# Performance work log

Hardware: AMD Instinct MI355X
Metric: run time of the kernel (lower is better)

The kernel has to match this reference:

```python
import jax, jax.numpy as jnp
import numpy as np

N = 100000   # nodes
D = 64       # in_features
E = 1200000  # edges (avg degree ~12)
C = 1.0      # curvature
MIN_NORM = 1e-15
PROJ_EPS = 4e-3  # float32 eps used by HGCN-style PoincareBall.proj


def setup_inputs() -> dict:
    key = jax.random.key(0)
    k1, k2, k3 = jax.random.split(key, 3)
    x = jax.random.normal(k1, (N, D), dtype=jnp.float32) * 0.1
    edge_index = jax.random.randint(k2, (2, E), 0, N, dtype=jnp.int32)
    # GCNConv learned params (lin weight + bias)
    W = jax.random.normal(k3, (D, D), dtype=jnp.float32) / np.sqrt(D)
    b = jnp.zeros((D,), dtype=jnp.float32)
    return {"x": x, "W": W, "b": b, "edge_index": edge_index}


def expmap0(u, c):
    sqrt_c = jnp.sqrt(c)
    u_norm = jnp.maximum(jnp.linalg.norm(u, axis=-1, keepdims=True), MIN_NORM)
    return jnp.tanh(sqrt_c * u_norm) * u / (sqrt_c * u_norm)


def proj(x, c):
    norm = jnp.maximum(jnp.linalg.norm(x, axis=-1, keepdims=True), MIN_NORM)
    maxnorm = (1.0 - PROJ_EPS) / jnp.sqrt(c)
    return jnp.where(norm > maxnorm, x / norm * maxnorm, x)


def gcn_conv(x, W, b, edge_index, n_nodes):
    # PyG GCNConv: h = x @ W; add self-loops; symmetric normalization; scatter-add; + bias
    h = x @ W  # [N, D]
    src, dst = edge_index[0], edge_index[1]
    loops = jnp.arange(n_nodes, dtype=edge_index.dtype)
    s = jnp.concatenate([src, loops])  # [E+N]
    d = jnp.concatenate([dst, loops])
    deg = jax.ops.segment_sum(jnp.ones(s.shape, dtype=h.dtype), d, num_segments=n_nodes)
    deg_inv_sqrt = jnp.where(deg > 0, deg ** -0.5, 0.0)
    norm = deg_inv_sqrt[s] * deg_inv_sqrt[d]  # [E+N]
    msgs = h[s] * norm[:, None]               # gather + scale: [E+N, D]
    out = jax.ops.segment_sum(msgs, d, num_segments=n_nodes)  # scatter-add
    return out + b


def reference(x, W, b, edge_index):
    # Note: original computes logmap0(x) but discards it (conv uses raw x) -- dead code.
    support_t = gcn_conv(x, W, b, edge_index, N)
    return proj(expmap0(support_t, C), C)
```

## Files before the change

kernel.cpp:

```cpp
#include <hip/hip_runtime.h>
#include <hip/hip_bf16.h>

#define DFEAT 64
#define NBSH  8
#define NPB   256
#define EPB   2048
#define EPT   (EPB / 256)
#define CAPB  3584
#define REGS  4608

__global__ __launch_bounds__(256) void part_kernel(const int* __restrict__ ei,
                                                   int* __restrict__ deg,
                                                   int* __restrict__ bcnt,
                                                   unsigned* __restrict__ ebuf, int E) {
    __shared__ int h[512];
    __shared__ int base[512];
    int t = threadIdx.x;
    h[t] = 0; h[t + 256] = 0;
    __syncthreads();
    int bb = blockIdx.x * EPB;
    int sv[EPT], dv[EPT];
    #pragma unroll
    for (int i = 0; i < EPT; ++i) {
        int e = bb + i * 256 + t;
        if (e < E) {
            sv[i] = ei[e];
            dv[i] = ei[E + e];
            atomicAdd(&h[dv[i] >> NBSH], 1);
            atomicAdd(&deg[dv[i]], 1);
        } else dv[i] = -1;
    }
    __syncthreads();
    base[t]       = h[t]       ? atomicAdd(&bcnt[t],       h[t])       : 0;
    base[t + 256] = h[t + 256] ? atomicAdd(&bcnt[t + 256], h[t + 256]) : 0;
    __syncthreads();
    h[t] = 0; h[t + 256] = 0;
    __syncthreads();
    #pragma unroll
    for (int i = 0; i < EPT; ++i) {
        if (dv[i] >= 0) {
            int bkt = dv[i] >> NBSH;
            int pos = base[bkt] + atomicAdd(&h[bkt], 1);
            if (pos < CAPB)
                ebuf[(size_t)bkt * REGS + pos] =
                    (unsigned)sv[i] | ((unsigned)(dv[i] & (NPB - 1)) << 17);
        }
    }
}

__global__ __launch_bounds__(256) void prep_kernel(const int* __restrict__ deg,
                                                   const int* __restrict__ bcnt,
                                                   unsigned* __restrict__ buf,
                                                   int* __restrict__ begs,
                                                   int* __restrict__ lens,
                                                   float* __restrict__ dinv,
                                                   const float* __restrict__ x,
                                                   unsigned* __restrict__ xs,
                                                   int n, int nbuck) {
    __shared__ unsigned eb[CAPB];
    __shared__ int tmp[256];
    __shared__ int cnt[256];
    int t = threadIdx.x;

    if ((int)blockIdx.x >= nbuck) {
        int i = ((int)blockIdx.x - nbuck) * 256 + t;
        int total = (n + 1) * 32;
        if (i >= total) return;
        int row = i >> 5, col = i & 31;
        unsigned v = 0;
        if (row < n) {
            float di = rsqrtf((float)(deg[row] + 1));
            if (col == 0) dinv[row] = di;
            float f0 = x[(size_t)row * DFEAT + 2 * col] * di;
            float f1 = x[(size_t)row * DFEAT + 2 * col + 1] * di;
            unsigned u0 = __float_as_uint(f0); u0 = (u0 + 0x7fffu + ((u0 >> 16) & 1u)) >> 16;
            unsigned u1 = __float_as_uint(f1); u1 = (u1 + 0x7fffu + ((u1 >> 16) & 1u)) >> 16;
            v = (u0 & 0xffffu) | (u1 << 16);
        }
        xs[i] = v;
        return;
    }

    int b = blockIdx.x;
    size_t rb = (size_t)b * REGS;
    int ecnt = bcnt[b]; if (ecnt > CAPB) ecnt = CAPB;

    const uint4* bufv = (const uint4*)(buf + rb);
    uint4* ebv = (uint4*)eb;
    int nv = (ecnt + 3) >> 2;
    for (int i = t; i < nv; i += 256) ebv[i] = bufv[i];

    int nid = (b << NBSH) + t;
    int d = (nid < n) ? deg[nid] : 0;
    int slots = (nid < n) ? ((d + 4) & ~3) : 0;
    tmp[t] = slots;
    __syncthreads();
    int s = slots;
    for (int o = 1; o < 256; o <<= 1) {
        int y = (t >= o) ? tmp[t - o] : 0;
        __syncthreads();
        tmp[t] += y;
        __syncthreads();
    }
    int excl = tmp[t] - s;
    int beg = (int)rb + excl;
    if (nid < n) {
        begs[nid] = beg;
        lens[nid] = slots;
        buf[beg] = (unsigned)nid;
        for (int k = d + 1; k < slots; ++k) buf[beg + k] = (unsigned)n;
    }
    cnt[t] = excl + 1;
    __syncthreads();
    for (int i = t; i < ecnt; i += 256) {
        unsigned v = eb[i];
        int pos = atomicAdd(&cnt[v >> 17], 1);
        buf[rb + pos] = v & 0x1ffffu;
    }
}

__global__ __launch_bounds__(256) void agg_kernel(const int* __restrict__ begs,
                                                  const int* __restrict__ lens,
                                                  const int* __restrict__ srcs,
                                                  const float* __restrict__ dinv,
                                                  const uint2* __restrict__ xs2,
                                                  const float* __restrict__ W,
                                                  const float* __restrict__ b,
                                                  float* __restrict__ out,
                                                  int n, int noctets) {
    __shared__ float Wl[DFEAT * DFEAT];
    __shared__ float xl[8][DFEAT];
    int t = threadIdx.x;
    #pragma unroll
    for (int i = 0; i < 16; ++i) Wl[i * 256 + t] = W[i * 256 + t];
    __syncthreads();

    int r = t >> 6, lane = t & 63;
    int g = lane >> 4;
    int q = lane & 15;
    float bias = b[lane];

    for (int oct = blockIdx.x; oct < noctets; oct += gridDim.x) {
        int na = oct * 8 + r;
        int nb_ = na + 4;
        bool va = na < n, vb = nb_ < n;
        if (!va) continue;

        int beg0 = begs[na],  end0 = beg0 + lens[na];
        int beg1 = 0, end1 = 0;
        if (vb) { beg1 = begs[nb_]; end1 = beg1 + lens[nb_]; }

        float a0 = 0, a1 = 0, a2 = 0, a3 = 0;
        float b0 = 0, b1 = 0, b2 = 0, b3 = 0;
        int base0 = beg0, base1 = beg1;
        while (base0 < end0 || base1 < end1) {
            int m0 = end0 - base0; m0 = m0 < 0 ? 0 : (m0 > 64 ? 64 : m0);
            int m1 = end1 - base1; m1 = m1 < 0 ? 0 : (m1 > 64 ? 64 : m1);
            int idx0 = 0, idx1 = 0;
            if (lane < m0) idx0 = srcs[base0 + lane];
            if (lane < m1) idx1 = srcs[base1 + lane];
            int q0 = m0 >> 2, q1 = m1 >> 2;
            int qc = q0 < q1 ? q0 : q1;
            #pragma unroll 4
            for (int j = 0; j < qc; ++j) {
                int sv0 = __shfl(idx0, 4 * j + g, 64);
                int sv1 = __shfl(idx1, 4 * j + g, 64);
                uint2 d0 = xs2[(unsigned)sv0 * 16 + q];
                uint2 d1 = xs2[(unsigned)sv1 * 16 + q];
                a0 += __uint_as_float(d0.x << 16);
                a1 += __uint_as_float(d0.x & 0xffff0000u);
                a2 += __uint_as_float(d0.y << 16);
                a3 += __uint_as_float(d0.y & 0xffff0000u);
                b0 += __uint_as_float(d1.x << 16);
                b1 += __uint_as_float(d1.x & 0xffff0000u);
                b2 += __uint_as_float(d1.y << 16);
                b3 += __uint_as_float(d1.y & 0xffff0000u);
            }
            #pragma unroll 4
            for (int j = qc; j < q0; ++j) {
                int sv0 = __shfl(idx0, 4 * j + g, 64);
                uint2 d0 = xs2[(unsigned)sv0 * 16 + q];
                a0 += __uint_as_float(d0.x << 16);
                a1 += __uint_as_float(d0.x & 0xffff0000u);
                a2 += __uint_as_float(d0.y << 16);
                a3 += __uint_as_float(d0.y & 0xffff0000u);
            }
            #pragma unroll 4
            for (int j = qc; j < q1; ++j) {
                int sv1 = __shfl(idx1, 4 * j + g, 64);
                uint2 d1 = xs2[(unsigned)sv1 * 16 + q];
                b0 += __uint_as_float(d1.x << 16);
                b1 += __uint_as_float(d1.x & 0xffff0000u);
                b2 += __uint_as_float(d1.y << 16);
                b3 += __uint_as_float(d1.y & 0xffff0000u);
            }
            base0 += 64; base1 += 64;
        }
        #pragma unroll
        for (int off = 16; off < 64; off <<= 1) {
            a0 += __shfl_xor(a0, off, 64);
            a1 += __shfl_xor(a1, off, 64);
            a2 += __shfl_xor(a2, off, 64);
            a3 += __shfl_xor(a3, off, 64);
            b0 += __shfl_xor(b0, off, 64);
            b1 += __shfl_xor(b1, off, 64);
            b2 += __shfl_xor(b2, off, 64);
            b3 += __shfl_xor(b3, off, 64);
        }
        if (g == 0) {
            float dia = dinv[na];
            xl[r][4 * q + 0] = a0 * dia;
            xl[r][4 * q + 1] = a1 * dia;
            xl[r][4 * q + 2] = a2 * dia;
            xl[r][4 * q + 3] = a3 * dia;
            if (vb) {
                float dib = dinv[nb_];
                xl[r + 4][4 * q + 0] = b0 * dib;
                xl[r + 4][4 * q + 1] = b1 * dib;
                xl[r + 4][4 * q + 2] = b2 * dib;
                xl[r + 4][4 * q + 3] = b3 * dib;
            }
        }

        float oa0 = bias, oa1 = 0.0f, ob0 = bias, ob1 = 0.0f;
        #pragma unroll
        for (int k = 0; k < DFEAT; k += 2) {
            float w0 = Wl[k * DFEAT + lane];
            float w1 = Wl[(k + 1) * DFEAT + lane];
            oa0 = fmaf(xl[r][k],     w0, oa0);
            oa1 = fmaf(xl[r][k + 1], w1, oa1);
            ob0 = fmaf(xl[r + 4][k],     w0, ob0);
            ob1 = fmaf(xl[r + 4][k + 1], w1, ob1);
        }
        float oa = oa0 + oa1;
        float ob = ob0 + ob1;

        float ssa = oa * oa, ssb = ob * ob;
        #pragma unroll
        for (int off = 32; off > 0; off >>= 1) {
            ssa += __shfl_xor(ssa, off, 64);
            ssb += __shfl_xor(ssb, off, 64);
        }
        float norma = fmaxf(sqrtf(ssa), 1e-15f);
        float sca = fminf(tanhf(norma), 1.0f - 4e-3f) / norma;
        out[(long long)na * DFEAT + lane] = oa * sca;
        if (vb) {
            float normb = fmaxf(sqrtf(ssb), 1e-15f);
            float scb = fminf(tanhf(normb), 1.0f - 4e-3f) / normb;
            out[(long long)nb_ * DFEAT + lane] = ob * scb;
        }
    }
}


extern "C" void kernel_launch(void* const* d_in, const int* in_sizes, int n_in,
                              void* d_out, int out_size, void* d_ws, size_t ws_size,
                              hipStream_t stream) {
    const float* x = (const float*)d_in[0];
    const float* W = (const float*)d_in[1];
    const float* b = (const float*)d_in[2];
    const int* ei  = (const int*)d_in[3];

    int n = in_sizes[0] / DFEAT;
    int E = in_sizes[3] / 2;
    int NBUCK = (n + NPB - 1) / NPB;
    int nblk = (E + EPB - 1) / EPB;
    int noctets = (n + 7) / 8;
    int np = (n + 3) & ~3;

    int* deg  = (int*)d_ws;
    int* bcnt = deg + np;
    unsigned* buf = (unsigned*)(bcnt + 512);
    int* begs = (int*)(buf + (size_t)NBUCK * REGS);
    int* lens = begs + n;
    float* dinv = (float*)(lens + n);
    size_t xsoff = (size_t)(((int*)dinv + n) - (int*)d_ws);
    xsoff = (xsoff + 31) & ~(size_t)31;
    unsigned* xs = (unsigned*)d_ws + xsoff;

    float* out = (float*)d_out;

    int aggblocks = 2048;
    if (aggblocks > noctets) aggblocks = noctets;
    int xsblocks = ((n + 1) * 32 + 255) / 256;

    hipMemsetAsync(deg, 0, (size_t)(np + 512) * sizeof(int), stream);
    part_kernel<<<nblk, 256, 0, stream>>>(ei, deg, bcnt, buf, E);
    prep_kernel<<<NBUCK + xsblocks, 256, 0, stream>>>(deg, bcnt, buf, begs, lens,
                                                      dinv, x, xs, n, NBUCK);
    agg_kernel <<<aggblocks, 256, 0, stream>>>(begs, lens, (const int*)buf, dinv,
                                               (const uint2*)xs, W, b, out, n, noctets);
}
```

Measured before the change: 220.9 us.

## Compute node degrees from bucketed edges in shared memory instead of global atomics

Drops the per-edge global atomicAdd on the degree array in the partition kernel. Degrees are now counted in the CSR-build kernel with shared-memory atomics over each bucket's staged edges, and dinv is written there. The scaled bf16 feature conversion moves into a separate kernel that runs after dinv is ready, adding one launch, and the degree memset shrinks. If a bucket overflows CAPB, degrees are taken from the truncated edge list rather than the full one.

```diff
diff --git a/kernel.cpp b/kernel.cpp
--- a/kernel.cpp
+++ b/kernel.cpp
@@ -10,7 +10,6 @@
 #define REGS  4608
 
 __global__ __launch_bounds__(256) void part_kernel(const int* __restrict__ ei,
-                                                   int* __restrict__ deg,
                                                    int* __restrict__ bcnt,
                                                    unsigned* __restrict__ ebuf, int E) {
     __shared__ int h[512];
@@ -27,7 +26,6 @@
             sv[i] = ei[e];
             dv[i] = ei[E + e];
             atomicAdd(&h[dv[i] >> NBSH], 1);
-            atomicAdd(&deg[dv[i]], 1);
         } else dv[i] = -1;
     }
     __syncthreads();
@@ -48,51 +46,30 @@
     }
 }
 
-__global__ __launch_bounds__(256) void prep_kernel(const int* __restrict__ deg,
-                                                   const int* __restrict__ bcnt,
-                                                   unsigned* __restrict__ buf,
-                                                   int* __restrict__ begs,
-                                                   int* __restrict__ lens,
-                                                   float* __restrict__ dinv,
-                                                   const float* __restrict__ x,
-                                                   unsigned* __restrict__ xs,
-                                                   int n, int nbuck) {
+__global__ __launch_bounds__(256) void csr_kernel(const int* __restrict__ bcnt,
+                                                  unsigned* __restrict__ buf,
+                                                  int* __restrict__ begs,
+                                                  int* __restrict__ lens,
+                                                  float* __restrict__ dinv, int n) {
     __shared__ unsigned eb[CAPB];
+    __shared__ int cnt[256];
     __shared__ int tmp[256];
-    __shared__ int cnt[256];
-    int t = threadIdx.x;
-
-    if ((int)blockIdx.x >= nbuck) {
-        int i = ((int)blockIdx.x - nbuck) * 256 + t;
-        int total = (n + 1) * 32;
-        if (i >= total) return;
-        int row = i >> 5, col = i & 31;
-        unsigned v = 0;
-        if (row < n) {
-            float di = rsqrtf((float)(deg[row] + 1));
-            if (col == 0) dinv[row] = di;
-            float f0 = x[(size_t)row * DFEAT + 2 * col] * di;
-            float f1 = x[(size_t)row * DFEAT + 2 * col + 1] * di;
-            unsigned u0 = __float_as_uint(f0); u0 = (u0 + 0x7fffu + ((u0 >> 16) & 1u)) >> 16;
-            unsigned u1 = __float_as_uint(f1); u1 = (u1 + 0x7fffu + ((u1 >> 16) & 1u)) >> 16;
-            v = (u0 & 0xffffu) | (u1 << 16);
-        }
-        xs[i] = v;
-        return;
-    }
-
-    int b = blockIdx.x;
+    int t = threadIdx.x, b = blockIdx.x;
+    int ecnt = bcnt[b]; if (ecnt > CAPB) ecnt = CAPB;
     size_t rb = (size_t)b * REGS;
-    int ecnt = bcnt[b]; if (ecnt > CAPB) ecnt = CAPB;
 
     const uint4* bufv = (const uint4*)(buf + rb);
     uint4* ebv = (uint4*)eb;
     int nv = (ecnt + 3) >> 2;
     for (int i = t; i < nv; i += 256) ebv[i] = bufv[i];
+    cnt[t] = 0;
+    __syncthreads();
+    for (int i = t; i < ecnt; i += 256) atomicAdd(&cnt[eb[i] >> 17], 1);
+    __syncthreads();
 
     int nid = (b << NBSH) + t;
-    int d = (nid < n) ? deg[nid] : 0;
-    int slots = (nid < n) ? ((d + 4) & ~3) : 0;
+    int deg = cnt[t];
+    int slots = (nid < n) ? ((deg + 4) & ~3) : 0;
     tmp[t] = slots;
     __syncthreads();
     int s = slots;
@@ -107,8 +84,9 @@
     if (nid < n) {
         begs[nid] = beg;
         lens[nid] = slots;
+        dinv[nid] = rsqrtf((float)(deg + 1));
         buf[beg] = (unsigned)nid;
-        for (int k = d + 1; k < slots; ++k) buf[beg + k] = (unsigned)n;
+        for (int k = deg + 1; k < slots; ++k) buf[beg + k] = (unsigned)n;
     }
     cnt[t] = excl + 1;
     __syncthreads();
@@ -117,6 +95,25 @@
         int pos = atomicAdd(&cnt[v >> 17], 1);
         buf[rb + pos] = v & 0x1ffffu;
     }
+}
+
+__global__ __launch_bounds__(256) void xsprep_kernel(const float* __restrict__ x,
+                                                     const float* __restrict__ dinv,
+                                                     unsigned* __restrict__ xs, int n) {
+    int i = blockIdx.x * blockDim.x + threadIdx.x;
+    int total = (n + 1) * 32;
+    if (i >= total) return;
+    int row = i >> 5, col = i & 31;
+    unsigned v = 0;
+    if (row < n) {
+        float di = dinv[row];
+        float f0 = x[(size_t)row * DFEAT + 2 * col] * di;
+        float f1 = x[(size_t)row * DFEAT + 2 * col + 1] * di;
+        unsigned u0 = __float_as_uint(f0); u0 = (u0 + 0x7fffu + ((u0 >> 16) & 1u)) >> 16;
+        unsigned u1 = __float_as_uint(f1); u1 = (u1 + 0x7fffu + ((u1 >> 16) & 1u)) >> 16;
+        v = (u0 & 0xffffu) | (u1 << 16);
+    }
+    xs[i] = v;
 }
 
 __global__ __launch_bounds__(256) void agg_kernel(const int* __restrict__ begs,
@@ -266,10 +263,8 @@
     int NBUCK = (n + NPB - 1) / NPB;
     int nblk = (E + EPB - 1) / EPB;
     int noctets = (n + 7) / 8;
-    int np = (n + 3) & ~3;
-
-    int* deg  = (int*)d_ws;
-    int* bcnt = deg + np;
+
+    int* bcnt = (int*)d_ws;
     unsigned* buf = (unsigned*)(bcnt + 512);
     int* begs = (int*)(buf + (size_t)NBUCK * REGS);
     int* lens = begs + n;
@@ -284,10 +279,10 @@
     if (aggblocks > noctets) aggblocks = noctets;
     int xsblocks = ((n + 1) * 32 + 255) / 256;
 
-    hipMemsetAsync(deg, 0, (size_t)(np + 512) * sizeof(int), stream);
-    part_kernel<<<nblk, 256, 0, stream>>>(ei, deg, bcnt, buf, E);
-    prep_kernel<<<NBUCK + xsblocks, 256, 0, stream>>>(deg, bcnt, buf, begs, lens,
-                                                      dinv, x, xs, n, NBUCK);
-    agg_kernel <<<aggblocks, 256, 0, stream>>>(begs, lens, (const int*)buf, dinv,
-                                               (const uint2*)xs, W, b, out, n, noctets);
-}
+    hipMemsetAsync(bcnt, 0, 512 * sizeof(int), stream);
+    part_kernel  <<<nblk, 256, 0, stream>>>(ei, bcnt, buf, E);
+    csr_kernel   <<<NBUCK, 256, 0, stream>>>(bcnt, buf, begs, lens, dinv, n);
+    xsprep_kernel<<<xsblocks, 256, 0, stream>>>(x, dinv, xs, n);
+    agg_kernel   <<<aggblocks, 256, 0, stream>>>(begs, lens, (const int*)buf, dinv,
+                                                 (const uint2*)xs, W, b, out, n, noctets);
+}
```

Measured after the change: 185.5 us. -16.0%, faster.
